# Performance work log

Measured on AMD Instinct MI355X. Metric: run time of the kernel, lower is better.

## Reference

```python
import jax, jax.numpy as jnp
import numpy as np

NEG_BIG = -9e15  # matches torch's -9000000000000000.0 mask value


def setup_inputs() -> dict:
    key = jax.random.key(0)
    k0, k1, k2, k3 = jax.random.split(key, 4)
    B, N, F_IN, F_OUT = 8, 2048, 128, 128
    h = jax.random.normal(k0, (B, N, F_IN), dtype=jnp.float32)
    adj = jax.random.randint(k1, (B, N, N), 0, 2, dtype=jnp.int32)
    W = jax.random.normal(k2, (F_IN, F_OUT), dtype=jnp.float32) * 0.05
    a = jax.random.normal(k3, (2 * F_OUT,), dtype=jnp.float32) * 0.05
    return {"h": h, "adj": adj, "W": W, "a": a}


def reference(h, adj, W, a):
    # Wh: [B, N, F_out]
    Wh = jnp.einsum("bnf,fo->bno", h, W)
    f_out = Wh.shape[-1]
    # a @ [Wh_i || Wh_j] == (a1 @ Wh_i) + (a2 @ Wh_j): avoids O(N^2 * 2F) concat
    a1, a2 = a[:f_out], a[f_out:]
    src = jnp.einsum("bno,o->bn", Wh, a1)  # row (i) contribution
    dst = jnp.einsum("bno,o->bn", Wh, a2)  # col (j) contribution
    e = jax.nn.leaky_relu(src[:, :, None] + dst[:, None, :], negative_slope=0.2)
    e = jnp.where(adj > 0, e, NEG_BIG)
    attention = jax.nn.softmax(e, axis=-1)  # dropout is identity at eval time
    h_prime = jnp.einsum("bij,bjo->bio", attention, Wh)
    return h_prime
```

## Files before the change

### kernel.cpp

```cpp
#include <hip/hip_runtime.h>
#include <hip/hip_bf16.h>

#define BB 8
#define NN 2048
#define FF 128

typedef __bf16 bf16x8 __attribute__((ext_vector_type(8)));
typedef float f32x4 __attribute__((ext_vector_type(4)));

__device__ __forceinline__ void gload_lds16(const void* g, void* l) {
    __builtin_amdgcn_global_load_lds(
        (const __attribute__((address_space(1))) unsigned int*)g,
        (__attribute__((address_space(3))) unsigned int*)l, 16, 0, 0);
}

__global__ __launch_bounds__(256) void wh_kernel(
    const float* __restrict__ h, const float* __restrict__ W,
    const float* __restrict__ a, __bf16* __restrict__ fragB,
    float* __restrict__ srcg, float* __restrict__ dstg)
{
    __shared__ float  s_h[32][132];
    __shared__ __bf16 s_wh[32][132];
    __shared__ float  s_s[2][32];
    __shared__ float  s_d[2][32];

    const int bid = blockIdx.x;
    const int b   = bid >> 6;
    const int J   = bid & 63;
    const int r0  = J * 32;
    const int t   = threadIdx.x;
    const int w   = t >> 6;
    const int l   = t & 63;
    const int itile = w & 1;
    const int fh    = w >> 1;
    const int g     = l >> 4;
    const int c16   = l & 15;

#pragma unroll
    for (int i = 0; i < 4; ++i) {
        const int idx = t + i * 256;
        const int r   = idx >> 5;
        const int c4  = idx & 31;
        *(f32x4*)&s_h[r][c4 * 4] =
            *(const f32x4*)(h + (size_t)(b * NN + r0 + r) * FF + c4 * 4);
    }
    __syncthreads();

    const float* hrow = &s_h[itile * 16 + c16][0];

    f32x4 acc[4] = {};

#pragma unroll
    for (int kt = 0; kt < 4; ++kt) {
        const int k0 = kt * 32 + g * 8;
        f32x4 h0 = *(const f32x4*)(hrow + k0);
        f32x4 h1 = *(const f32x4*)(hrow + k0 + 4);
        bf16x8 af;
        af[0]=(__bf16)h0[0]; af[1]=(__bf16)h0[1]; af[2]=(__bf16)h0[2]; af[3]=(__bf16)h0[3];
        af[4]=(__bf16)h1[0]; af[5]=(__bf16)h1[1]; af[6]=(__bf16)h1[2]; af[7]=(__bf16)h1[3];
#pragma unroll
        for (int ft = 0; ft < 4; ++ft) {
            const int c = (fh * 4 + ft) * 16 + c16;
            bf16x8 bf;
#pragma unroll
            for (int e = 0; e < 8; ++e) bf[e] = (__bf16)W[(k0 + e) * FF + c];
            acc[ft] = __builtin_amdgcn_mfma_f32_16x16x32_bf16(af, bf, acc[ft], 0, 0, 0);
        }
    }

    float a1v[4], a2v[4];
#pragma unroll
    for (int ft = 0; ft < 4; ++ft) {
        const int c = (fh * 4 + ft) * 16 + c16;
        a1v[ft] = a[c];
        a2v[ft] = a[FF + c];
    }
#pragma unroll
    for (int r = 0; r < 4; ++r) {
        float s = 0.f, d2 = 0.f;
#pragma unroll
        for (int ft = 0; ft < 4; ++ft) {
            s  += acc[ft][r] * a1v[ft];
            d2 += acc[ft][r] * a2v[ft];
        }
#pragma unroll
        for (int m = 1; m <= 8; m <<= 1) {
            s  += __shfl_xor(s,  m);
            d2 += __shfl_xor(d2, m);
        }
        if (c16 == 0) {
            s_s[fh][itile * 16 + g * 4 + r] = s;
            s_d[fh][itile * 16 + g * 4 + r] = d2;
        }
    }

#pragma unroll
    for (int ft = 0; ft < 4; ++ft)
#pragma unroll
        for (int r = 0; r < 4; ++r)
            s_wh[itile * 16 + g * 4 + r][(fh * 4 + ft) * 16 + c16] = (__bf16)acc[ft][r];

    __syncthreads();

#pragma unroll
    for (int e2 = 0; e2 < 2; ++e2) {
        const int ent  = t + e2 * 256;
        const int ftE  = ent >> 6;
        const int lE   = ent & 63;
        const int rowE = (lE >> 4) * 8;
        const int colE = ftE * 16 + (lE & 15);
        bf16x8 v;
#pragma unroll
        for (int ee = 0; ee < 8; ++ee) v[ee] = s_wh[rowE + ee][colE];
        *(bf16x8*)(fragB + ((size_t)((b * 64 + J) * 8 + ftE) * 64 + lE) * 8) = v;
    }

    if (t < 32) {
        srcg[b * NN + r0 + t] = s_s[0][t] + s_s[1][t];
        dstg[b * NN + r0 + t] = s_d[0][t] + s_d[1][t];
    }
}

__global__ __launch_bounds__(256, 2) void attn_kernel(
    const int* __restrict__ adj, const __bf16* __restrict__ fragB,
    const float* __restrict__ srcg, const float* __restrict__ dstg,
    float* __restrict__ out)
{
    __shared__ char  s_pipe[65536];
    __shared__ float s_dst[NN];
    __shared__ float s_ps[2][64];

    const int bid0 = blockIdx.x;
    const int bid  = (bid0 & 7) * 64 + (bid0 >> 3);
    const int b    = bid >> 6;
    const int I0   = (bid & 63) * 32;
    const int t    = threadIdx.x;
    const int w    = t >> 6;
    const int l    = t & 63;
    const int it   = w >> 1;
    const int h    = w & 1;
    const int g    = l >> 4;
    const int c16  = l & 15;

    {
        const f32x4* gs = (const f32x4*)(dstg + (size_t)b * NN);
        ((f32x4*)s_dst)[t]       = gs[t];
        ((f32x4*)s_dst)[t + 256] = gs[t + 256];
    }

    const char* adjB  = (const char*)adj;
    const size_t rA0  = (size_t)(b * NN + I0 + it * 16 + (l >> 3)) * (NN * 4)
                        + h * 128 + 16 * ((l & 7) ^ (l >> 3));
    const char* aSrc0 = adjB + rA0;
    const char* aSrc1 = adjB + rA0 + (size_t)8 * NN * 4;
    char* aDst0 = s_pipe + (w * 2 + 0) * 1024;
    char* aDst1 = s_pipe + (w * 2 + 1) * 1024;

    const char* fragBB = (const char*)fragB + (size_t)b * 524288;
    const char* fSrc0 = fragBB + ((w*4+0) >> 3) * 8192 + ((w*4+0) & 7) * 1024 + l * 16;
    const char* fSrc1 = fragBB + ((w*4+1) >> 3) * 8192 + ((w*4+1) & 7) * 1024 + l * 16;
    const char* fSrc2 = fragBB + ((w*4+2) >> 3) * 8192 + ((w*4+2) & 7) * 1024 + l * 16;
    const char* fSrc3 = fragBB + ((w*4+3) >> 3) * 8192 + ((w*4+3) & 7) * 1024 + l * 16;
    char* fDst0 = s_pipe + 32768 + (w*4+0) * 1024;
    char* fDst1 = s_pipe + 32768 + (w*4+1) * 1024;
    char* fDst2 = s_pipe + 32768 + (w*4+2) * 1024;
    char* fDst3 = s_pipe + 32768 + (w*4+3) * 1024;

#define STAGE_A(kA_, sl_) {                                                   \
        gload_lds16(aSrc0 + (size_t)(kA_) * 256, aDst0 + (sl_) * 8192);       \
        gload_lds16(aSrc1 + (size_t)(kA_) * 256, aDst1 + (sl_) * 8192); }
#define STAGE_F(kF_, sl_) {                                                   \
        gload_lds16(fSrc0 + (size_t)(kF_) * 16384, fDst0 + (sl_) * 16384);    \
        gload_lds16(fSrc1 + (size_t)(kF_) * 16384, fDst1 + (sl_) * 16384);    \
        gload_lds16(fSrc2 + (size_t)(kF_) * 16384, fDst2 + (sl_) * 16384);    \
        gload_lds16(fSrc3 + (size_t)(kF_) * 16384, fDst3 + (sl_) * 16384); }

    STAGE_A(0, 0);
    STAGE_A(1, 1);
    STAGE_F(0, 0);
    STAGE_A(2, 2);

    const float sv = srcg[b * NN + I0 + it * 16 + c16];
    const int   sw = (c16 & 7) << 4;

    f32x4 acc[8] = {};
    float psum = 0.f;

    for (int kt = 0; kt < 32; ++kt) {
        asm volatile("s_waitcnt vmcnt(2) lgkmcnt(0)" ::: "memory");
        __builtin_amdgcn_s_barrier();
        asm volatile("" ::: "memory");

        const int kF = (kt + 1) & 31;
        const int kA = (kt + 3) & 31;
        STAGE_F(kF, (kt + 1) & 1);
        STAGE_A(kA, (kt + 3) & 3);

        const char* atile = s_pipe + (kt & 3) * 8192 + w * 2048 + c16 * 128;
        const int4 A0 = *(const int4*)(atile + ((g * 32)      ^ sw));
        const int4 A1 = *(const int4*)(atile + ((g * 32 + 16) ^ sw));
        const int j0 = kt * 64 + h * 32 + g * 8;
        const f32x4 d0 = *(const f32x4*)(s_dst + j0);
        const f32x4 d1 = *(const f32x4*)(s_dst + j0 + 4);
        const int   am[8] = {A0.x, A0.y, A0.z, A0.w, A1.x, A1.y, A1.z, A1.w};
        const float dv[8] = {d0[0], d0[1], d0[2], d0[3], d1[0], d1[1], d1[2], d1[3]};

        bf16x8 af;
#pragma unroll
        for (int e = 0; e < 8; ++e) {
            float x = sv + dv[e];
            x = fmaxf(x, 0.2f * x);
            float p = __expf(x);
            p = (am[e] > 0) ? p : 0.f;
            psum += p;
            af[e] = (__bf16)p;
        }

        const char* ftile = s_pipe + 32768 + (kt & 1) * 16384 + h * 8192 + l * 16;
#pragma unroll
        for (int ft = 0; ft < 8; ++ft) {
            const bf16x8 bf = *(const bf16x8*)(ftile + ft * 1024);
            acc[ft] = __builtin_amdgcn_mfma_f32_16x16x32_bf16(af, bf, acc[ft], 0, 0, 0);
        }
    }

    psum += __shfl_xor(psum, 16);
    psum += __shfl_xor(psum, 32);

    __syncthreads();
    float* s_comb = (float*)s_pipe;
    if (h == 1) {
        float* cb = s_comb + (it * 64 + l) * 33;
#pragma unroll
        for (int ft = 0; ft < 8; ++ft)
#pragma unroll
            for (int r = 0; r < 4; ++r) cb[ft * 4 + r] = acc[ft][r];
        s_ps[it][l] = psum;
    }
    __syncthreads();
    if (h == 0) {
        psum += s_ps[it][l];
        const float* cb = s_comb + (it * 64 + l) * 33;
#pragma unroll
        for (int ft = 0; ft < 8; ++ft)
#pragma unroll
            for (int r = 0; r < 4; ++r) acc[ft][r] += cb[ft * 4 + r];

#pragma unroll
        for (int r = 0; r < 4; ++r) {
            const float dinv = 1.f / __shfl(psum, g * 4 + r);
            const int row = I0 + it * 16 + g * 4 + r;
            float* orow = out + (size_t)(b * NN + row) * FF + c16;
#pragma unroll
            for (int ft = 0; ft < 8; ++ft) orow[ft * 16] = acc[ft][r] * dinv;
        }
    }
#undef STAGE_A
#undef STAGE_F
}

extern "C" void kernel_launch(void* const* d_in, const int* in_sizes, int n_in,
                              void* d_out, int out_size, void* d_ws, size_t ws_size,
                              hipStream_t stream)
{
    const float* h   = (const float*)d_in[0];
    const int*   adj = (const int*)d_in[1];
    const float* W   = (const float*)d_in[2];
    const float* a   = (const float*)d_in[3];
    float* out = (float*)d_out;

    char* ws = (char*)d_ws;
    __bf16* fragB = (__bf16*)ws;
    float*  srcg  = (float*)(ws + (4 << 20));
    float*  dstg  = (float*)(ws + (4 << 20) + (64 << 10));

    wh_kernel<<<512, 256, 0, stream>>>(h, W, a, fragB, srcg, dstg);
    attn_kernel<<<512, 256, 0, stream>>>(adj, fragB, srcg, dstg, out);
}
```

Before: 44.17 us.

## Pack adjacency into bitmap in prep kernel and deepen fragB pipeline

Adds 4096 blocks to the prep kernel that compress the int32 adjacency matrix into a 1-bit-per-entry bitmap. The attention kernel then reads one mask byte per step instead of staging adjacency tiles in LDS, and uses the freed LDS to quadruple-buffer the Wh fragment tiles. The loop is unrolled with explicit vmcnt accounting. The full adjacency matrix is still read once in the prep kernel, so the gain relies on better overlap and on the attention kernel becoming lighter.

Result: slower. 58.81 us (+33.2%).

```diff
diff --git a/kernel.cpp b/kernel.cpp
--- a/kernel.cpp
+++ b/kernel.cpp
@@ -14,23 +14,45 @@
         (__attribute__((address_space(3))) unsigned int*)l, 16, 0, 0);
 }
 
-__global__ __launch_bounds__(256) void wh_kernel(
-    const float* __restrict__ h, const float* __restrict__ W,
-    const float* __restrict__ a, __bf16* __restrict__ fragB,
-    float* __restrict__ srcg, float* __restrict__ dstg)
+__global__ __launch_bounds__(256) void prep_kernel(
+    const float* __restrict__ h, const int* __restrict__ adj,
+    const float* __restrict__ W, const float* __restrict__ a,
+    __bf16* __restrict__ fragB, float* __restrict__ srcg,
+    float* __restrict__ dstg, unsigned char* __restrict__ bmp)
 {
     __shared__ float  s_h[32][132];
     __shared__ __bf16 s_wh[32][132];
     __shared__ float  s_s[2][32];
     __shared__ float  s_d[2][32];
 
-    const int bid = blockIdx.x;
+    const int bidr = blockIdx.x;
+    const int t    = threadIdx.x;
+    const int w    = t >> 6;
+    const int l    = t & 63;
+
+    if (bidr < 4096) {
+        const int row = bidr * 4 + w;
+        const int* ar = adj + (size_t)row * NN;
+        unsigned char* br = bmp + (size_t)row * 256;
+#pragma unroll
+        for (int i = 0; i < 4; ++i) {
+            const int j0 = i * 512 + l * 8;
+            const int4 v0 = *(const int4*)(ar + j0);
+            const int4 v1 = *(const int4*)(ar + j0 + 4);
+            const unsigned byte =
+                  (unsigned)(v0.x > 0)        | ((unsigned)(v0.y > 0) << 1)
+                | ((unsigned)(v0.z > 0) << 2) | ((unsigned)(v0.w > 0) << 3)
+                | ((unsigned)(v1.x > 0) << 4) | ((unsigned)(v1.y > 0) << 5)
+                | ((unsigned)(v1.z > 0) << 6) | ((unsigned)(v1.w > 0) << 7);
+            br[i * 64 + l] = (unsigned char)byte;
+        }
+        return;
+    }
+
+    const int bid = bidr - 4096;
     const int b   = bid >> 6;
     const int J   = bid & 63;
     const int r0  = J * 32;
-    const int t   = threadIdx.x;
-    const int w   = t >> 6;
-    const int l   = t & 63;
     const int itile = w & 1;
     const int fh    = w >> 1;
     const int g     = l >> 4;
@@ -47,7 +69,6 @@
     __syncthreads();
 
     const float* hrow = &s_h[itile * 16 + c16][0];
-
     f32x4 acc[4] = {};
 
 #pragma unroll
@@ -122,7 +143,7 @@
 }
 
 __global__ __launch_bounds__(256, 2) void attn_kernel(
-    const int* __restrict__ adj, const __bf16* __restrict__ fragB,
+    const unsigned char* __restrict__ bmp, const __bf16* __restrict__ fragB,
     const float* __restrict__ srcg, const float* __restrict__ dstg,
     float* __restrict__ out)
 {
@@ -142,87 +163,84 @@
     const int g    = l >> 4;
     const int c16  = l & 15;
 
+    const float sv = srcg[b * NN + I0 + it * 16 + c16];
+
     {
-        const f32x4* gs = (const f32x4*)(dstg + (size_t)b * NN);
-        ((f32x4*)s_dst)[t]       = gs[t];
-        ((f32x4*)s_dst)[t + 256] = gs[t + 256];
-    }
-
-    const char* adjB  = (const char*)adj;
-    const size_t rA0  = (size_t)(b * NN + I0 + it * 16 + (l >> 3)) * (NN * 4)
-                        + h * 128 + 16 * ((l & 7) ^ (l >> 3));
-    const char* aSrc0 = adjB + rA0;
-    const char* aSrc1 = adjB + rA0 + (size_t)8 * NN * 4;
-    char* aDst0 = s_pipe + (w * 2 + 0) * 1024;
-    char* aDst1 = s_pipe + (w * 2 + 1) * 1024;
+        const char* dsrc = (const char*)(dstg + (size_t)b * NN) + w * 2048 + l * 16;
+        char* ddst = (char*)s_dst + w * 2048;
+        gload_lds16(dsrc,        ddst);
+        gload_lds16(dsrc + 1024, ddst + 1024);
+    }
 
     const char* fragBB = (const char*)fragB + (size_t)b * 524288;
-    const char* fSrc0 = fragBB + ((w*4+0) >> 3) * 8192 + ((w*4+0) & 7) * 1024 + l * 16;
-    const char* fSrc1 = fragBB + ((w*4+1) >> 3) * 8192 + ((w*4+1) & 7) * 1024 + l * 16;
-    const char* fSrc2 = fragBB + ((w*4+2) >> 3) * 8192 + ((w*4+2) & 7) * 1024 + l * 16;
-    const char* fSrc3 = fragBB + ((w*4+3) >> 3) * 8192 + ((w*4+3) & 7) * 1024 + l * 16;
-    char* fDst0 = s_pipe + 32768 + (w*4+0) * 1024;
-    char* fDst1 = s_pipe + 32768 + (w*4+1) * 1024;
-    char* fDst2 = s_pipe + 32768 + (w*4+2) * 1024;
-    char* fDst3 = s_pipe + 32768 + (w*4+3) * 1024;
-
-#define STAGE_A(kA_, sl_) {                                                   \
-        gload_lds16(aSrc0 + (size_t)(kA_) * 256, aDst0 + (sl_) * 8192);       \
-        gload_lds16(aSrc1 + (size_t)(kA_) * 256, aDst1 + (sl_) * 8192); }
-#define STAGE_F(kF_, sl_) {                                                   \
-        gload_lds16(fSrc0 + (size_t)(kF_) * 16384, fDst0 + (sl_) * 16384);    \
-        gload_lds16(fSrc1 + (size_t)(kF_) * 16384, fDst1 + (sl_) * 16384);    \
-        gload_lds16(fSrc2 + (size_t)(kF_) * 16384, fDst2 + (sl_) * 16384);    \
-        gload_lds16(fSrc3 + (size_t)(kF_) * 16384, fDst3 + (sl_) * 16384); }
-
-    STAGE_A(0, 0);
-    STAGE_A(1, 1);
-    STAGE_F(0, 0);
-    STAGE_A(2, 2);
-
-    const float sv = srcg[b * NN + I0 + it * 16 + c16];
-    const int   sw = (c16 & 7) << 4;
+    const char* fS0 = fragBB + ((w*4+0) >> 3) * 8192 + ((w*4+0) & 7) * 1024 + l * 16;
+    const char* fS1 = fragBB + ((w*4+1) >> 3) * 8192 + ((w*4+1) & 7) * 1024 + l * 16;
+    const char* fS2 = fragBB + ((w*4+2) >> 3) * 8192 + ((w*4+2) & 7) * 1024 + l * 16;
+    const char* fS3 = fragBB + ((w*4+3) >> 3) * 8192 + ((w*4+3) & 7) * 1024 + l * 16;
+    char* fD0 = s_pipe + (w*4+0) * 1024;
+    char* fD1 = s_pipe + (w*4+1) * 1024;
+    char* fD2 = s_pipe + (w*4+2) * 1024;
+    char* fD3 = s_pipe + (w*4+3) * 1024;
+
+    const unsigned char* bp =
+        bmp + (size_t)(b * NN + I0 + it * 16 + c16) * 256 + h * 4 + g;
+
+#define STAGE_G(kt_, BT_) {                                                   \
+        const int sl_ = (kt_) & 3;                                            \
+        gload_lds16(fS0 + (size_t)(kt_) * 16384, fD0 + sl_ * 16384);          \
+        gload_lds16(fS1 + (size_t)(kt_) * 16384, fD1 + sl_ * 16384);          \
+        gload_lds16(fS2 + (size_t)(kt_) * 16384, fD2 + sl_ * 16384);          \
+        gload_lds16(fS3 + (size_t)(kt_) * 16384, fD3 + sl_ * 16384);          \
+        asm volatile("global_load_ubyte %0, %1, off"                          \
+                     : "=&v"(BT_) : "v"(bp + (size_t)(kt_) * 8)); }
+
+#define STEPC(kt_, BT_) {                                                     \
+        const int j0_ = (kt_) * 64 + h * 32 + g * 8;                          \
+        const f32x4 d0_ = *(const f32x4*)(s_dst + j0_);                       \
+        const f32x4 d1_ = *(const f32x4*)(s_dst + j0_ + 4);                   \
+        const float dv_[8] = {d0_[0], d0_[1], d0_[2], d0_[3],                 \
+                              d1_[0], d1_[1], d1_[2], d1_[3]};                \
+        const unsigned msk_ = BT_;                                            \
+        bf16x8 af_;                                                           \
+        _Pragma("unroll")                                                     \
+        for (int e = 0; e < 8; ++e) {                                         \
+            float x = sv + dv_[e];                                            \
+            x = fmaxf(x, 0.2f * x);                                           \
+            float p = __expf(x);                                              \
+            p = ((msk_ >> e) & 1u) ? p : 0.f;                                 \
+            psum += p;                                                        \
+            af_[e] = (__bf16)p;                                               \
+        }                                                                     \
+        const char* ftile_ = s_pipe + ((kt_) & 3) * 16384 + h * 8192 + l * 16;\
+        _Pragma("unroll")                                                     \
+        for (int ft = 0; ft < 8; ++ft) {                                      \
+            const bf16x8 bf_ = *(const bf16x8*)(ftile_ + ft * 1024);          \
+            acc[ft] = __builtin_amdgcn_mfma_f32_16x16x32_bf16(af_, bf_, acc[ft], 0, 0, 0); \
+        } }
+
+#define BARRIER_W(VMC_) {                                                     \
+        asm volatile("s_waitcnt vmcnt(" VMC_ ") lgkmcnt(0)" ::: "memory");    \
+        __builtin_amdgcn_s_barrier();                                         \
+        asm volatile("" ::: "memory"); }
 
     f32x4 acc[8] = {};
     float psum = 0.f;
-
-    for (int kt = 0; kt < 32; ++kt) {
-        asm volatile("s_waitcnt vmcnt(2) lgkmcnt(0)" ::: "memory");
-        __builtin_amdgcn_s_barrier();
-        asm volatile("" ::: "memory");
-
-        const int kF = (kt + 1) & 31;
-        const int kA = (kt + 3) & 31;
-        STAGE_F(kF, (kt + 1) & 1);
-        STAGE_A(kA, (kt + 3) & 3);
-
-        const char* atile = s_pipe + (kt & 3) * 8192 + w * 2048 + c16 * 128;
-        const int4 A0 = *(const int4*)(atile + ((g * 32)      ^ sw));
-        const int4 A1 = *(const int4*)(atile + ((g * 32 + 16) ^ sw));
-        const int j0 = kt * 64 + h * 32 + g * 8;
-        const f32x4 d0 = *(const f32x4*)(s_dst + j0);
-        const f32x4 d1 = *(const f32x4*)(s_dst + j0 + 4);
-        const int   am[8] = {A0.x, A0.y, A0.z, A0.w, A1.x, A1.y, A1.z, A1.w};
-        const float dv[8] = {d0[0], d0[1], d0[2], d0[3], d1[0], d1[1], d1[2], d1[3]};
-
-        bf16x8 af;
-#pragma unroll
-        for (int e = 0; e < 8; ++e) {
-            float x = sv + dv[e];
-            x = fmaxf(x, 0.2f * x);
-            float p = __expf(x);
-            p = (am[e] > 0) ? p : 0.f;
-            psum += p;
-            af[e] = (__bf16)p;
-        }
-
-        const char* ftile = s_pipe + 32768 + (kt & 1) * 16384 + h * 8192 + l * 16;
-#pragma unroll
-        for (int ft = 0; ft < 8; ++ft) {
-            const bf16x8 bf = *(const bf16x8*)(ftile + ft * 1024);
-            acc[ft] = __builtin_amdgcn_mfma_f32_16x16x32_bf16(af, bf, acc[ft], 0, 0, 0);
-        }
-    }
+    unsigned bt[4];
+
+    STAGE_G(0, bt[0]);
+    STAGE_G(1, bt[1]);
+    STAGE_G(2, bt[2]);
+
+#pragma unroll 4
+    for (int kt = 0; kt < 28; ++kt) {
+        BARRIER_W("10")
+        STAGE_G(kt + 3, bt[(kt + 3) & 3]);
+        STEPC(kt, bt[kt & 3]);
+    }
+    BARRIER_W("10")  STAGE_G(31, bt[3]);  STEPC(28, bt[0]);
+    BARRIER_W("10")  STEPC(29, bt[1]);
+    BARRIER_W("5")   STEPC(30, bt[2]);
+    BARRIER_W("0")   STEPC(31, bt[3]);
 
     psum += __shfl_xor(psum, 16);
     psum += __shfl_xor(psum, 32);
@@ -255,8 +273,9 @@
             for (int ft = 0; ft < 8; ++ft) orow[ft * 16] = acc[ft][r] * dinv;
         }
     }
-#undef STAGE_A
-#undef STAGE_F
+#undef STAGE_G
+#undef STEPC
+#undef BARRIER_W
 }
 
 extern "C" void kernel_launch(void* const* d_in, const int* in_sizes, int n_in,
@@ -270,10 +289,11 @@
     float* out = (float*)d_out;
 
     char* ws = (char*)d_ws;
-    __bf16* fragB = (__bf16*)ws;
-    float*  srcg  = (float*)(ws + (4 << 20));
-    float*  dstg  = (float*)(ws + (4 << 20) + (64 << 10));
-
-    wh_kernel<<<512, 256, 0, stream>>>(h, W, a, fragB, srcg, dstg);
-    attn_kernel<<<512, 256, 0, stream>>>(adj, fragB, srcg, dstg, out);
-}
+    __bf16*        fragB = (__bf16*)ws;
+    unsigned char* bmp   = (unsigned char*)(ws + (4 << 20));
+    float* srcg = (float*)(ws + (8 << 20));
+    float* dstg = (float*)(ws + (8 << 20) + (64 << 10));
+
+    prep_kernel<<<4608, 256, 0, stream>>>(h, adj, W, a, fragB, srcg, dstg, bmp);
+    attn_kernel<<<512, 256, 0, stream>>>(bmp, fragB, srcg, dstg, out);
+}
```
